# Kernel tuning notes

Hardware: AMD Instinct MI355X
Metric: run time of the kernel (lower is better)

The kernel has to match this reference:

```python
import jax, jax.numpy as jnp
import numpy as np
from jax import lax

N = 100000
N_CLASSES = 16
N_EDGES = 3200000
LAYERS = 4
ALPHA = 0.5


def setup_inputs() -> dict:
    key = jax.random.key(0)
    k1, k2, k3, k4 = jax.random.split(key, 4)
    x = jax.random.uniform(k1, (N, N_CLASSES), dtype=jnp.float32)
    W = jnp.ones((1, N), dtype=jnp.float32)
    edge_weight = jax.random.uniform(k2, (N_EDGES,), dtype=jnp.float32)
    degree = jax.random.uniform(k3, (N,), dtype=jnp.float32)
    edge_index = jax.random.randint(k4, (2, N_EDGES), 0, N, dtype=jnp.int32)
    return {"x": x, "W": W, "edge_weight": edge_weight, "degree": degree,
            "edge_index": edge_index}


def reference(x, W, edge_weight, degree, edge_index):
    # degree -> (N,1), squared
    deg2 = (degree * degree)[:, None]
    w_node = W.reshape(-1, 1)          # per-node weight (N,1)
    src = edge_index[0]
    dst = edge_index[1]
    ew = edge_weight[:, None]

    def layer(h, _):
        new_h = w_node * h                                  # elementwise scale
        msgs = new_h[src] * ew                              # (E, C) gather+scale
        agg = jax.ops.segment_sum(msgs, dst, num_segments=N)  # sparse adj matmul
        new_h = deg2 * agg                                  # degree reweight
        new_h = ALPHA * h + (1.0 - ALPHA) * new_h           # residual blend
        new_h = new_h / jnp.sum(new_h, axis=1, keepdims=True)  # row normalize
        return new_h, None

    x, _ = lax.scan(layer, x, None, length=LAYERS)
    return x
```

## Files before the change

### kernel.cpp

```cpp
#include <hip/hip_runtime.h>

#define NN 100000
#define NC 16
#define NE 3200000
#define NLAYERS 4
#define ALPHA_C 0.5f

#define BSHIFT 8
#define NBUK 391
#define EPB 12544
#define NBLK 256
#define CAP 12288
#define LCAP 4096

typedef __attribute__((ext_vector_type(4))) _Float16 half4;
typedef __attribute__((ext_vector_type(8))) _Float16 half8;

static __device__ __forceinline__ unsigned short f2h_bits(float w) {
    _Float16 h = (_Float16)w;
    unsigned short b;
    __builtin_memcpy(&b, &h, 2);
    return b;
}
static __device__ __forceinline__ float hbits2f(unsigned short b) {
    _Float16 h;
    __builtin_memcpy(&h, &b, 2);
    return (float)h;
}


__global__ __launch_bounds__(1024) void bucket_count(const int* __restrict__ dst,
                                                     int* __restrict__ counts,
                                                     const float* __restrict__ x,
                                                     _Float16* __restrict__ h16) {
    __shared__ int h[NBUK];
    for (int i = threadIdx.x; i < NBUK; i += 1024) h[i] = 0;
    __syncthreads();
    int base = blockIdx.x * EPB;
    int nedge = min(EPB, NE - base);
    for (int i = threadIdx.x; i < nedge; i += 1024)
        atomicAdd(&h[dst[base + i] >> BSHIFT], 1);
    __syncthreads();
    for (int i = threadIdx.x; i < NBUK; i += 1024)
        counts[i * NBLK + blockIdx.x] = h[i];
    for (int i = blockIdx.x * 1024 + threadIdx.x; i < NN * NC / 4; i += NBLK * 1024) {
        float4 v = *reinterpret_cast<const float4*>(x + i * 4);
        half4 o;
        o.x = (_Float16)v.x; o.y = (_Float16)v.y;
        o.z = (_Float16)v.z; o.w = (_Float16)v.w;
        *reinterpret_cast<half4*>(h16 + i * 4) = o;
    }
}

__global__ void scanA(int* __restrict__ data, int* __restrict__ blockSums, int n) {
    __shared__ int lds[256];
    int base = blockIdx.x * 1024 + threadIdx.x * 4;
    int v[4] = {0, 0, 0, 0};
#pragma unroll
    for (int i = 0; i < 4; ++i) { int idx = base + i; if (idx < n) v[i] = data[idx]; }
    int tsum = v[0] + v[1] + v[2] + v[3];
    lds[threadIdx.x] = tsum;
    __syncthreads();
    for (int off = 1; off < 256; off <<= 1) {
        int t = (threadIdx.x >= off) ? lds[threadIdx.x - off] : 0;
        __syncthreads();
        lds[threadIdx.x] += t;
        __syncthreads();
    }
    if (threadIdx.x == 255) blockSums[blockIdx.x] = lds[255];
    int run = lds[threadIdx.x] - tsum;
#pragma unroll
    for (int i = 0; i < 4; ++i) {
        int idx = base + i;
        if (idx < n) { int old = v[i]; data[idx] = run; run += old; }
    }
}

__global__ void scanB(int* __restrict__ blockSums, int nb) {
    __shared__ int lds[1024];
    int t = threadIdx.x;
    lds[t] = (t < nb) ? blockSums[t] : 0;
    __syncthreads();
    for (int off = 1; off < 1024; off <<= 1) {
        int v = (t >= off) ? lds[t - off] : 0;
        __syncthreads();
        lds[t] += v;
        __syncthreads();
    }
    if (t < nb) blockSums[t] = (t == 0) ? 0 : lds[t - 1];
}

__global__ __launch_bounds__(1024) void bucket_scatter(
        const int* __restrict__ src, const int* __restrict__ dst,
        const float* __restrict__ ew, const float* __restrict__ W,
        const int* __restrict__ counts, const int* __restrict__ blockSums,
        unsigned* __restrict__ payload4, unsigned char* __restrict__ lbid1) {
    __shared__ unsigned lpay[EPB];
    __shared__ unsigned short lbid[EPB];
    __shared__ unsigned char ldst[EPB];
    __shared__ int h[NBUK];
    __shared__ int lbase[NBUK];
    __shared__ int delta[NBUK];
    __shared__ int sc[512];
    int t = threadIdx.x;
    int blk = blockIdx.x;
    for (int i = t; i < NBUK; i += 1024) h[i] = 0;
    __syncthreads();
    int base = blk * EPB;
    int nedge = min(EPB, NE - base);
    for (int i = t; i < nedge; i += 1024)
        atomicAdd(&h[dst[base + i] >> BSHIFT], 1);
    __syncthreads();
    if (t < 512) sc[t] = (t < NBUK) ? h[t] : 0;
    __syncthreads();
    for (int off = 1; off < 512; off <<= 1) {
        int v = (t >= off && t < 512) ? sc[t - off] : 0;
        __syncthreads();
        if (t < 512) sc[t] += v;
        __syncthreads();
    }
    if (t < NBUK) {
        int excl = sc[t] - h[t];
        lbase[t] = excl;
        int gidx = t * NBLK + blk;
        delta[t] = counts[gidx] + blockSums[gidx >> 10] - excl;
        h[t] = 0;
    }
    __syncthreads();
    for (int i = t; i < nedge; i += 1024) {
        int e = base + i;
        int d = dst[e];
        int s = src[e];
        float w = ew[e] * W[s];
        int b = d >> BSHIFT;
        int r = atomicAdd(&h[b], 1);
        int slot = lbase[b] + r;
        unsigned short hb = f2h_bits(w);
        lpay[slot] = (unsigned)s | ((unsigned)hb << 17);
        lbid[slot] = (unsigned short)b;
        ldst[slot] = (unsigned char)(d & 255);
    }
    __syncthreads();
    for (int i = t; i < nedge; i += 1024) {
        int b = lbid[i];
        int pos = i + delta[b];
        payload4[pos] = lpay[i];
        lbid1[pos] = ldst[i];
    }
}

__global__ void bucket_sort(const unsigned* __restrict__ payload4,
                            const unsigned char* __restrict__ lbid1,
                            unsigned* __restrict__ recs4,
                            const int* __restrict__ counts,
                            const int* __restrict__ blockSums,
                            int* __restrict__ offsets) {
    __shared__ unsigned lpay[CAP];
    __shared__ unsigned char lld[CAP];
    __shared__ int hcnt[256];
    __shared__ int hscan[256];
    __shared__ int hexcl[256];
    int b = blockIdx.x;
    int t = threadIdx.x;
    int i0 = b * NBLK;
    int beg = counts[i0] + blockSums[i0 >> 10];
    int end;
    if (b == NBUK - 1) end = NE;
    else {
        int i1 = (b + 1) * NBLK;
        end = counts[i1] + blockSums[i1 >> 10];
    }
    int cnt = end - beg;
    if (t < 256) hcnt[t] = 0;
    __syncthreads();
    for (int i = t; i < cnt && i < CAP; i += 512) {
        lpay[i] = payload4[beg + i];
        int ld = lbid1[beg + i];
        lld[i] = (unsigned char)ld;
        atomicAdd(&hcnt[ld], 1);
    }
    __syncthreads();
    if (t < 256) hscan[t] = hcnt[t];
    __syncthreads();
    for (int off = 1; off < 256; off <<= 1) {
        int v = 0;
        if (t >= off && t < 256) v = hscan[t - off];
        __syncthreads();
        if (t < 256) hscan[t] += v;
        __syncthreads();
    }
    if (t < 256) {
        hexcl[t] = hscan[t] - hcnt[t];
        int d = (b << BSHIFT) + t;
        if (d < NN) offsets[d] = beg + hexcl[t];
        hcnt[t] = 0;
    }
    if (b == NBUK - 1 && t == 0) offsets[NN] = NE;
    __syncthreads();
    for (int i = t; i < cnt && i < CAP; i += 512) {
        int ld = lld[i];
        int r = atomicAdd(&hcnt[ld], 1);
        recs4[beg + hexcl[ld] + r] = lpay[i];
    }
}

template<bool LAST>
__global__ __launch_bounds__(256, 8) void gather_f16(
        const _Float16* __restrict__ h, const unsigned* __restrict__ recs,
        const int* __restrict__ offsets, const float* __restrict__ degree,
        _Float16* __restrict__ hout16, float* __restrict__ hout32) {
    __shared__ unsigned lrec[LCAP];
    __shared__ int srange[2];
    int tid = threadIdx.x;
    int gfirst = blockIdx.x * 32;
    if (tid < 2) srange[tid] = offsets[gfirst + tid * 32];
    __syncthreads();
    int beg0 = srange[0];
    int n0 = srange[1] - beg0;
    bool staged = (n0 <= LCAP);
    if (staged) {
        for (int i = tid; i < n0; i += 256)
            lrec[i] = recs[beg0 + i];
    }
    __syncthreads();
    int g = gfirst + (tid >> 3);
    int sub = tid & 7;
    int q8 = (sub & 1) * 8;
    int quarter = sub >> 1;
    int beg = offsets[g];
    int end = offsets[g + 1];
    int len = end - beg;
    int qlen = (len + 3) >> 2;
    int lo = beg + quarter * qlen;
    int hi = lo + qlen;
    if (lo > end) lo = end;
    if (hi > end) hi = end;
    float acc[8] = {0.f, 0.f, 0.f, 0.f, 0.f, 0.f, 0.f, 0.f};
    if (staged) {
        int i = lo - beg0;
        int hh = hi - beg0;
        for (; i + 4 <= hh; i += 4) {
            unsigned r0 = lrec[i];
            unsigned r1 = lrec[i + 1];
            unsigned r2 = lrec[i + 2];
            unsigned r3 = lrec[i + 3];
            int s0 = r0 & 0x1FFFF, s1 = r1 & 0x1FFFF, s2 = r2 & 0x1FFFF, s3 = r3 & 0x1FFFF;
            const half8 h0 = *reinterpret_cast<const half8*>(h + (size_t)s0 * NC + q8);
            const half8 h1 = *reinterpret_cast<const half8*>(h + (size_t)s1 * NC + q8);
            const half8 h2 = *reinterpret_cast<const half8*>(h + (size_t)s2 * NC + q8);
            const half8 h3 = *reinterpret_cast<const half8*>(h + (size_t)s3 * NC + q8);
            float w0 = hbits2f((unsigned short)(r0 >> 17));
            float w1 = hbits2f((unsigned short)(r1 >> 17));
            float w2 = hbits2f((unsigned short)(r2 >> 17));
            float w3 = hbits2f((unsigned short)(r3 >> 17));
#pragma unroll
            for (int j = 0; j < 8; ++j) {
                acc[j] += (float)h0[j] * w0 + (float)h1[j] * w1
                        + (float)h2[j] * w2 + (float)h3[j] * w3;
            }
        }
        for (; i < hh; ++i) {
            unsigned r0 = lrec[i];
            int s0 = r0 & 0x1FFFF;
            float w0 = hbits2f((unsigned short)(r0 >> 17));
            const half8 h0 = *reinterpret_cast<const half8*>(h + (size_t)s0 * NC + q8);
#pragma unroll
            for (int j = 0; j < 8; ++j) acc[j] += (float)h0[j] * w0;
        }
    } else {
        int i = lo;
        for (; i + 4 <= hi; i += 4) {
            unsigned r0 = __builtin_nontemporal_load(recs + i);
            unsigned r1 = __builtin_nontemporal_load(recs + i + 1);
            unsigned r2 = __builtin_nontemporal_load(recs + i + 2);
            unsigned r3 = __builtin_nontemporal_load(recs + i + 3);
            int s0 = r0 & 0x1FFFF, s1 = r1 & 0x1FFFF, s2 = r2 & 0x1FFFF, s3 = r3 & 0x1FFFF;
            const half8 h0 = *reinterpret_cast<const half8*>(h + (size_t)s0 * NC + q8);
            const half8 h1 = *reinterpret_cast<const half8*>(h + (size_t)s1 * NC + q8);
            const half8 h2 = *reinterpret_cast<const half8*>(h + (size_t)s2 * NC + q8);
            const half8 h3 = *reinterpret_cast<const half8*>(h + (size_t)s3 * NC + q8);
            float w0 = hbits2f((unsigned short)(r0 >> 17));
            float w1 = hbits2f((unsigned short)(r1 >> 17));
            float w2 = hbits2f((unsigned short)(r2 >> 17));
            float w3 = hbits2f((unsigned short)(r3 >> 17));
#pragma unroll
            for (int j = 0; j < 8; ++j) {
                acc[j] += (float)h0[j] * w0 + (float)h1[j] * w1
                        + (float)h2[j] * w2 + (float)h3[j] * w3;
            }
        }
        for (; i < hi; ++i) {
            unsigned r0 = __builtin_nontemporal_load(recs + i);
            int s0 = r0 & 0x1FFFF;
            float w0 = hbits2f((unsigned short)(r0 >> 17));
            const half8 h0 = *reinterpret_cast<const half8*>(h + (size_t)s0 * NC + q8);
#pragma unroll
            for (int j = 0; j < 8; ++j) acc[j] += (float)h0[j] * w0;
        }
    }
#pragma unroll
    for (int j = 0; j < 8; ++j) {
        acc[j] += __shfl_xor(acc[j], 2);
        acc[j] += __shfl_xor(acc[j], 4);
    }
    float deg = degree[g];
    float d2 = deg * deg;
    const half8 hsv = *reinterpret_cast<const half8*>(h + (size_t)g * NC + q8);
    float v[8];
    float s8 = 0.f;
#pragma unroll
    for (int j = 0; j < 8; ++j) {
        v[j] = ALPHA_C * (float)hsv[j] + (1.f - ALPHA_C) * d2 * acc[j];
        s8 += v[j];
    }
    s8 += __shfl_xor(s8, 1);
    float inv = 1.f / s8;
#pragma unroll
    for (int j = 0; j < 8; ++j) v[j] *= inv;
    if (quarter == 0) {
        if (LAST) {
            float4 o0 = make_float4(v[0], v[1], v[2], v[3]);
            float4 o1 = make_float4(v[4], v[5], v[6], v[7]);
            *reinterpret_cast<float4*>(hout32 + (size_t)g * NC + q8) = o0;
            *reinterpret_cast<float4*>(hout32 + (size_t)g * NC + q8 + 4) = o1;
        } else {
            half8 o;
#pragma unroll
            for (int j = 0; j < 8; ++j) o[j] = (_Float16)v[j];
            *reinterpret_cast<half8*>(hout16 + (size_t)g * NC + q8) = o;
        }
    }
}


__global__ void hist_kernel(const int* __restrict__ dst, int* __restrict__ counts) {
    int e = blockIdx.x * blockDim.x + threadIdx.x;
    if (e < NE) atomicAdd(&counts[dst[e]], 1);
}

__global__ void scanC_fb(int* __restrict__ data, const int* __restrict__ blockSums, int n) {
    int idx = blockIdx.x * blockDim.x + threadIdx.x;
    if (idx < n) data[idx] += blockSums[idx >> 10];
    if (idx == 0) data[n] = NE;
}

__global__ void scatter_sort(const int* __restrict__ src, const int* __restrict__ dst,
                             const float* __restrict__ ew, const float* __restrict__ W,
                             const int* __restrict__ offsets, int* __restrict__ cursor,
                             int2* __restrict__ sorted) {
    int e = blockIdx.x * blockDim.x + threadIdx.x;
    if (e >= NE) return;
    int d = dst[e];
    int s = src[e];
    int pos = offsets[d] + atomicAdd(&cursor[d], 1);
    float w = ew[e] * W[s];
    sorted[pos] = make_int2(s, __float_as_int(w));
}

__global__ void gather1(const float* __restrict__ h, const int2* __restrict__ recs,
                        const int* __restrict__ offsets, const float* __restrict__ degree,
                        float* __restrict__ hout) {
    int t = blockIdx.x * blockDim.x + threadIdx.x;
    int g = t >> 2;
    int q = t & 3;
    if (g >= NN) return;
    int q4 = q * 4;
    int beg = offsets[g];
    int end = offsets[g + 1];
    float4 acc = make_float4(0.f, 0.f, 0.f, 0.f);
    for (int i = beg; i < end; ++i) {
        int2 r0 = recs[i];
        float w0 = __int_as_float(r0.y);
        const float4 h0 = *reinterpret_cast<const float4*>(h + (size_t)(r0.x & 0x1FFFF) * NC + q4);
        acc.x += h0.x * w0; acc.y += h0.y * w0; acc.z += h0.z * w0; acc.w += h0.w * w0;
    }
    float deg = degree[g];
    float d2 = deg * deg;
    const float4 hs = *reinterpret_cast<const float4*>(h + (size_t)g * NC + q4);
    float4 v;
    v.x = ALPHA_C * hs.x + (1.f - ALPHA_C) * d2 * acc.x;
    v.y = ALPHA_C * hs.y + (1.f - ALPHA_C) * d2 * acc.y;
    v.z = ALPHA_C * hs.z + (1.f - ALPHA_C) * d2 * acc.z;
    v.w = ALPHA_C * hs.w + (1.f - ALPHA_C) * d2 * acc.w;
    float s4 = v.x + v.y + v.z + v.w;
    s4 += __shfl_xor(s4, 1);
    s4 += __shfl_xor(s4, 2);
    float inv = 1.f / s4;
    v.x *= inv; v.y *= inv; v.z *= inv; v.w *= inv;
    *reinterpret_cast<float4*>(hout + (size_t)g * NC + q4) = v;
}


extern "C" void kernel_launch(void* const* d_in, const int* in_sizes, int n_in,
                              void* d_out, int out_size, void* d_ws, size_t ws_size,
                              hipStream_t stream)
{
    const float* x      = (const float*)d_in[0];
    const float* W      = (const float*)d_in[1];
    const float* ew     = (const float*)d_in[2];
    const float* degree = (const float*)d_in[3];
    const int*   eidx   = (const int*)d_in[4];
    const int* src = eidx;
    const int* dst = eidx + NE;
    float* out = (float*)d_out;

    const int gather_blocks = NN / 32;
    const int node_blocks4  = (NN * 4 + 255) / 256;
    const int edge_blocks   = (NE + 255) / 256;

    const size_t pay_elems    = (size_t)NE;
    const size_t lbid_bytes   = (size_t)NE;
    const size_t recs4_elems  = (size_t)NE;
    const size_t h16_elems    = (size_t)NN * NC;
    const size_t counts_elems = (size_t)NBUK * NBLK + 1;
    const size_t off_elems    = (size_t)NN + 1;
    const size_t need = pay_elems * 4 + lbid_bytes + recs4_elems * 4
                      + h16_elems * 2 * 2 + counts_elems * 4 + off_elems * 4
                      + 1024 * 4 + 128;

    if (ws_size >= need) {
        unsigned*      payload4  = (unsigned*)d_ws;
        unsigned*      recs4     = payload4 + pay_elems;
        _Float16*      h16a      = (_Float16*)(recs4 + recs4_elems);
        _Float16*      h16b      = h16a + h16_elems;
        unsigned char* lbid1     = (unsigned char*)(h16b + h16_elems);
        int*           counts    = (int*)(lbid1 + lbid_bytes);
        int*           offsets   = counts + counts_elems;
        int*           blockSums = offsets + off_elems;

        bucket_count<<<NBLK, 1024, 0, stream>>>(dst, counts, x, h16a);
        const int n_scan = NBUK * NBLK;
        const int NB = (n_scan + 1023) / 1024;
        scanA<<<NB, 256, 0, stream>>>(counts, blockSums, n_scan);
        scanB<<<1, 1024, 0, stream>>>(blockSums, NB);
        bucket_scatter<<<NBLK, 1024, 0, stream>>>(src, dst, ew, W, counts, blockSums,
                                                  payload4, lbid1);
        bucket_sort<<<NBUK, 512, 0, stream>>>(payload4, lbid1, recs4, counts,
                                              blockSums, offsets);

        gather_f16<false><<<gather_blocks, 256, 0, stream>>>(h16a, recs4, offsets, degree, h16b, nullptr);
        gather_f16<false><<<gather_blocks, 256, 0, stream>>>(h16b, recs4, offsets, degree, h16a, nullptr);
        gather_f16<false><<<gather_blocks, 256, 0, stream>>>(h16a, recs4, offsets, degree, h16b, nullptr);
        gather_f16<true ><<<gather_blocks, 256, 0, stream>>>(h16b, recs4, offsets, degree, nullptr, out);
        return;
    }

    {
        const size_t bufA_elems = (size_t)NN * NC;
        int2*  sorted    = (int2*)d_ws;
        float* bufA      = (float*)(sorted + NE);
        int*   offsets   = (int*)(bufA + bufA_elems);
        int*   cursor    = offsets + (NN + 1);
        int*   blockSums = cursor + NN;

        (void)hipMemsetAsync(offsets, 0, (size_t)(2 * NN + 1) * sizeof(int), stream);
        hist_kernel<<<edge_blocks, 256, 0, stream>>>(dst, offsets);
        const int NB = (NN + 1023) / 1024;
        scanA<<<NB, 256, 0, stream>>>(offsets, blockSums, NN);
        scanB<<<1, 1024, 0, stream>>>(blockSums, NB);
        scanC_fb<<<(NN + 255) / 256, 256, 0, stream>>>(offsets, blockSums, NN);
        scatter_sort<<<edge_blocks, 256, 0, stream>>>(src, dst, ew, W, offsets, cursor, sorted);

        const float* hin = x;
        float* houts[NLAYERS] = {bufA, out, bufA, out};
        for (int l = 0; l < NLAYERS; ++l) {
            gather1<<<node_blocks4, 256, 0, stream>>>(hin, sorted, offsets, degree, houts[l]);
            hin = houts[l];
        }
    }
}
```

Before: 149.2 us.

## Drop the separate bucket-count pass by sorting locally and gathering runs per bucket

Result: slower. 153.0 us (+2.5%).

```diff
diff --git a/kernel.cpp b/kernel.cpp
--- a/kernel.cpp
+++ b/kernel.cpp
@@ -29,78 +29,16 @@
 }
 
 
-__global__ __launch_bounds__(1024) void bucket_count(const int* __restrict__ dst,
-                                                     int* __restrict__ counts,
-                                                     const float* __restrict__ x,
-                                                     _Float16* __restrict__ h16) {
-    __shared__ int h[NBUK];
-    for (int i = threadIdx.x; i < NBUK; i += 1024) h[i] = 0;
-    __syncthreads();
-    int base = blockIdx.x * EPB;
-    int nedge = min(EPB, NE - base);
-    for (int i = threadIdx.x; i < nedge; i += 1024)
-        atomicAdd(&h[dst[base + i] >> BSHIFT], 1);
-    __syncthreads();
-    for (int i = threadIdx.x; i < NBUK; i += 1024)
-        counts[i * NBLK + blockIdx.x] = h[i];
-    for (int i = blockIdx.x * 1024 + threadIdx.x; i < NN * NC / 4; i += NBLK * 1024) {
-        float4 v = *reinterpret_cast<const float4*>(x + i * 4);
-        half4 o;
-        o.x = (_Float16)v.x; o.y = (_Float16)v.y;
-        o.z = (_Float16)v.z; o.w = (_Float16)v.w;
-        *reinterpret_cast<half4*>(h16 + i * 4) = o;
-    }
-}
-
-__global__ void scanA(int* __restrict__ data, int* __restrict__ blockSums, int n) {
-    __shared__ int lds[256];
-    int base = blockIdx.x * 1024 + threadIdx.x * 4;
-    int v[4] = {0, 0, 0, 0};
-#pragma unroll
-    for (int i = 0; i < 4; ++i) { int idx = base + i; if (idx < n) v[i] = data[idx]; }
-    int tsum = v[0] + v[1] + v[2] + v[3];
-    lds[threadIdx.x] = tsum;
-    __syncthreads();
-    for (int off = 1; off < 256; off <<= 1) {
-        int t = (threadIdx.x >= off) ? lds[threadIdx.x - off] : 0;
-        __syncthreads();
-        lds[threadIdx.x] += t;
-        __syncthreads();
-    }
-    if (threadIdx.x == 255) blockSums[blockIdx.x] = lds[255];
-    int run = lds[threadIdx.x] - tsum;
-#pragma unroll
-    for (int i = 0; i < 4; ++i) {
-        int idx = base + i;
-        if (idx < n) { int old = v[i]; data[idx] = run; run += old; }
-    }
-}
-
-__global__ void scanB(int* __restrict__ blockSums, int nb) {
-    __shared__ int lds[1024];
-    int t = threadIdx.x;
-    lds[t] = (t < nb) ? blockSums[t] : 0;
-    __syncthreads();
-    for (int off = 1; off < 1024; off <<= 1) {
-        int v = (t >= off) ? lds[t - off] : 0;
-        __syncthreads();
-        lds[t] += v;
-        __syncthreads();
-    }
-    if (t < nb) blockSums[t] = (t == 0) ? 0 : lds[t - 1];
-}
-
 __global__ __launch_bounds__(1024) void bucket_scatter(
         const int* __restrict__ src, const int* __restrict__ dst,
         const float* __restrict__ ew, const float* __restrict__ W,
-        const int* __restrict__ counts, const int* __restrict__ blockSums,
-        unsigned* __restrict__ payload4, unsigned char* __restrict__ lbid1) {
+        int* __restrict__ counts, int* __restrict__ runstart,
+        unsigned* __restrict__ payload4, unsigned char* __restrict__ lbid1,
+        const float* __restrict__ x, _Float16* __restrict__ h16) {
     __shared__ unsigned lpay[EPB];
-    __shared__ unsigned short lbid[EPB];
     __shared__ unsigned char ldst[EPB];
     __shared__ int h[NBUK];
     __shared__ int lbase[NBUK];
-    __shared__ int delta[NBUK];
     __shared__ int sc[512];
     int t = threadIdx.x;
     int blk = blockIdx.x;
@@ -122,8 +60,8 @@
     if (t < NBUK) {
         int excl = sc[t] - h[t];
         lbase[t] = excl;
-        int gidx = t * NBLK + blk;
-        delta[t] = counts[gidx] + blockSums[gidx >> 10] - excl;
+        counts[t * NBLK + blk] = h[t];
+        runstart[t * NBLK + blk] = base + excl;
         h[t] = 0;
     }
     __syncthreads();
@@ -137,50 +75,84 @@
         int slot = lbase[b] + r;
         unsigned short hb = f2h_bits(w);
         lpay[slot] = (unsigned)s | ((unsigned)hb << 17);
-        lbid[slot] = (unsigned short)b;
         ldst[slot] = (unsigned char)(d & 255);
     }
     __syncthreads();
     for (int i = t; i < nedge; i += 1024) {
-        int b = lbid[i];
-        int pos = i + delta[b];
-        payload4[pos] = lpay[i];
-        lbid1[pos] = ldst[i];
-    }
+        payload4[base + i] = lpay[i];
+        lbid1[base + i] = ldst[i];
+    }
+    for (int i = blk * 1024 + t; i < NN * NC / 4; i += NBLK * 1024) {
+        float4 v = *reinterpret_cast<const float4*>(x + i * 4);
+        half4 o;
+        o.x = (_Float16)v.x; o.y = (_Float16)v.y;
+        o.z = (_Float16)v.z; o.w = (_Float16)v.w;
+        *reinterpret_cast<half4*>(h16 + i * 4) = o;
+    }
+}
+
+__global__ void scanA2(const int* __restrict__ in, int* __restrict__ out,
+                       int* __restrict__ blockSums, int n) {
+    __shared__ int lds[256];
+    int base = blockIdx.x * 1024 + threadIdx.x * 4;
+    int v[4] = {0, 0, 0, 0};
+#pragma unroll
+    for (int i = 0; i < 4; ++i) { int idx = base + i; if (idx < n) v[i] = in[idx]; }
+    int tsum = v[0] + v[1] + v[2] + v[3];
+    lds[threadIdx.x] = tsum;
+    __syncthreads();
+    for (int off = 1; off < 256; off <<= 1) {
+        int t = (threadIdx.x >= off) ? lds[threadIdx.x - off] : 0;
+        __syncthreads();
+        lds[threadIdx.x] += t;
+        __syncthreads();
+    }
+    if (threadIdx.x == 255) blockSums[blockIdx.x] = lds[255];
+    int run = lds[threadIdx.x] - tsum;
+#pragma unroll
+    for (int i = 0; i < 4; ++i) {
+        int idx = base + i;
+        if (idx < n) { int old = v[i]; out[idx] = run; run += old; }
+    }
+}
+
+__global__ void scanB(int* __restrict__ blockSums, int nb) {
+    __shared__ int lds[1024];
+    int t = threadIdx.x;
+    lds[t] = (t < nb) ? blockSums[t] : 0;
+    __syncthreads();
+    for (int off = 1; off < 1024; off <<= 1) {
+        int v = (t >= off) ? lds[t - off] : 0;
+        __syncthreads();
+        lds[t] += v;
+        __syncthreads();
+    }
+    if (t < nb) blockSums[t] = (t == 0) ? 0 : lds[t - 1];
 }
 
 __global__ void bucket_sort(const unsigned* __restrict__ payload4,
                             const unsigned char* __restrict__ lbid1,
                             unsigned* __restrict__ recs4,
-                            const int* __restrict__ counts,
+                            const int* __restrict__ rawcnt,
+                            const int* __restrict__ runstart,
+                            const int* __restrict__ scanned,
                             const int* __restrict__ blockSums,
                             int* __restrict__ offsets) {
     __shared__ unsigned lpay[CAP];
     __shared__ unsigned char lld[CAP];
+    __shared__ int rlen[256];
+    __shared__ int rpos[256];
+    __shared__ int rsrc[256];
     __shared__ int hcnt[256];
     __shared__ int hscan[256];
     __shared__ int hexcl[256];
     int b = blockIdx.x;
     int t = threadIdx.x;
-    int i0 = b * NBLK;
-    int beg = counts[i0] + blockSums[i0 >> 10];
-    int end;
-    if (b == NBUK - 1) end = NE;
-    else {
-        int i1 = (b + 1) * NBLK;
-        end = counts[i1] + blockSums[i1 >> 10];
-    }
-    int cnt = end - beg;
-    if (t < 256) hcnt[t] = 0;
-    __syncthreads();
-    for (int i = t; i < cnt && i < CAP; i += 512) {
-        lpay[i] = payload4[beg + i];
-        int ld = lbid1[beg + i];
-        lld[i] = (unsigned char)ld;
-        atomicAdd(&hcnt[ld], 1);
-    }
-    __syncthreads();
-    if (t < 256) hscan[t] = hcnt[t];
+    if (t < 256) {
+        rlen[t] = rawcnt[b * NBLK + t];
+        rsrc[t] = runstart[b * NBLK + t];
+        hscan[t] = rlen[t];
+    }
     __syncthreads();
     for (int off = 1; off < 256; off <<= 1) {
         int v = 0;
@@ -189,6 +161,38 @@
         if (t < 256) hscan[t] += v;
         __syncthreads();
     }
+    if (t < 256) rpos[t] = hscan[t] - rlen[t];
+    __syncthreads();
+    int cnt = hscan[255];
+    int wid = t >> 6;
+    int lane = t & 63;
+    for (int r = wid; r < 256; r += 8) {
+        int len = rlen[r];
+        int sp = rsrc[r];
+        int dp = rpos[r];
+        for (int i = lane; i < len; i += 64) {
+            int d = dp + i;
+            if (d < CAP) {
+                lpay[d] = payload4[sp + i];
+                lld[d] = lbid1[sp + i];
+            }
+        }
+    }
+    if (t < 256) hcnt[t] = 0;
+    __syncthreads();
+    for (int i = t; i < cnt && i < CAP; i += 512)
+        atomicAdd(&hcnt[lld[i]], 1);
+    __syncthreads();
+    if (t < 256) hscan[t] = hcnt[t];
+    __syncthreads();
+    for (int off = 1; off < 256; off <<= 1) {
+        int v = 0;
+        if (t >= off && t < 256) v = hscan[t - off];
+        __syncthreads();
+        if (t < 256) hscan[t] += v;
+        __syncthreads();
+    }
+    int beg = scanned[b * NBLK] + blockSums[(b * NBLK) >> 10];
     if (t < 256) {
         hexcl[t] = hscan[t] - hcnt[t];
         int d = (b << BSHIFT) + t;
@@ -338,6 +342,30 @@
     if (e < NE) atomicAdd(&counts[dst[e]], 1);
 }
 
+__global__ void scanA(int* __restrict__ data, int* __restrict__ blockSums, int n) {
+    __shared__ int lds[256];
+    int base = blockIdx.x * 1024 + threadIdx.x * 4;
+    int v[4] = {0, 0, 0, 0};
+#pragma unroll
+    for (int i = 0; i < 4; ++i) { int idx = base + i; if (idx < n) v[i] = data[idx]; }
+    int tsum = v[0] + v[1] + v[2] + v[3];
+    lds[threadIdx.x] = tsum;
+    __syncthreads();
+    for (int off = 1; off < 256; off <<= 1) {
+        int t = (threadIdx.x >= off) ? lds[threadIdx.x - off] : 0;
+        __syncthreads();
+        lds[threadIdx.x] += t;
+        __syncthreads();
+    }
+    if (threadIdx.x == 255) blockSums[blockIdx.x] = lds[255];
+    int run = lds[threadIdx.x] - tsum;
+#pragma unroll
+    for (int i = 0; i < 4; ++i) {
+        int idx = base + i;
+        if (idx < n) { int old = v[i]; data[idx] = run; run += old; }
+    }
+}
+
 __global__ void scanC_fb(int* __restrict__ data, const int* __restrict__ blockSums, int n) {
     int idx = blockIdx.x * blockDim.x + threadIdx.x;
     if (idx < n) data[idx] += blockSums[idx >> 10];
@@ -408,15 +436,15 @@
     const int node_blocks4  = (NN * 4 + 255) / 256;
     const int edge_blocks   = (NE + 255) / 256;
 
-    const size_t pay_elems    = (size_t)NE;
-    const size_t lbid_bytes   = (size_t)NE;
+    const size_t pay_elems    = (size_t)NBLK * EPB;
+    const size_t lbid_bytes   = (size_t)NBLK * EPB;
     const size_t recs4_elems  = (size_t)NE;
     const size_t h16_elems    = (size_t)NN * NC;
-    const size_t counts_elems = (size_t)NBUK * NBLK + 1;
+    const size_t cnt_elems    = (size_t)NBUK * NBLK + 1;
     const size_t off_elems    = (size_t)NN + 1;
     const size_t need = pay_elems * 4 + lbid_bytes + recs4_elems * 4
-                      + h16_elems * 2 * 2 + counts_elems * 4 + off_elems * 4
-                      + 1024 * 4 + 128;
+                      + h16_elems * 2 * 2 + cnt_elems * 4 * 3
+                      + off_elems * 4 + 1024 * 4 + 256;
 
     if (ws_size >= need) {
         unsigned*      payload4  = (unsigned*)d_ws;
@@ -424,19 +452,20 @@
         _Float16*      h16a      = (_Float16*)(recs4 + recs4_elems);
         _Float16*      h16b      = h16a + h16_elems;
         unsigned char* lbid1     = (unsigned char*)(h16b + h16_elems);
-        int*           counts    = (int*)(lbid1 + lbid_bytes);
-        int*           offsets   = counts + counts_elems;
+        int*           rawcnt    = (int*)(lbid1 + lbid_bytes);
+        int*           scanned   = rawcnt + cnt_elems;
+        int*           runstart  = scanned + cnt_elems;
+        int*           offsets   = runstart + cnt_elems;
         int*           blockSums = offsets + off_elems;
 
-        bucket_count<<<NBLK, 1024, 0, stream>>>(dst, counts, x, h16a);
+        bucket_scatter<<<NBLK, 1024, 0, stream>>>(src, dst, ew, W, rawcnt, runstart,
+                                                  payload4, lbid1, x, h16a);
         const int n_scan = NBUK * NBLK;
         const int NB = (n_scan + 1023) / 1024;
-        scanA<<<NB, 256, 0, stream>>>(counts, blockSums, n_scan);
+        scanA2<<<NB, 256, 0, stream>>>(rawcnt, scanned, blockSums, n_scan);
         scanB<<<1, 1024, 0, stream>>>(blockSums, NB);
-        bucket_scatter<<<NBLK, 1024, 0, stream>>>(src, dst, ew, W, counts, blockSums,
-                                                  payload4, lbid1);
-        bucket_sort<<<NBUK, 512, 0, stream>>>(payload4, lbid1, recs4, counts,
-                                              blockSums, offsets);
+        bucket_sort<<<NBUK, 512, 0, stream>>>(payload4, lbid1, recs4, rawcnt,
+                                              runstart, scanned, blockSums, offsets);
 
         gather_f16<false><<<gather_blocks, 256, 0, stream>>>(h16a, recs4, offsets, degree, h16b, nullptr);
         gather_f16<false><<<gather_blocks, 256, 0, stream>>>(h16b, recs4, offsets, degree, h16a, nullptr);
```
